# Kernel optimization log

Hardware: AMD Instinct MI355X
Metric: run time of the kernel (lower is better)

Reference implementation:

```python
import jax, jax.numpy as jnp
import numpy as np

D_MODEL = 1024
D_FFN = 4096
H = 16
D_HEAD = D_MODEL // H
B, L = 2, 2048
EPS = 1e-6


def layer_norm(x, a, b):
    # Matches torch: std is unbiased (ddof=1), and divides by (std + eps)
    mean = jnp.mean(x, axis=-1, keepdims=True)
    var = jnp.sum((x - mean) ** 2, axis=-1, keepdims=True) / (x.shape[-1] - 1)
    std = jnp.sqrt(var)
    return (x - mean) / (std + EPS) * a + b


def setup_inputs() -> dict:
    key = jax.random.key(0)
    ks = jax.random.split(key, 10)
    s = 0.02
    x = jax.random.normal(ks[0], (B, L, D_MODEL), dtype=jnp.float32)
    mask = jnp.tril(jnp.ones((L, L), dtype=jnp.int32))[None, None]  # causal [1,1,L,L]
    return {
        "x": x,
        "mask": mask,
        "Wqkv": jax.random.normal(ks[1], (D_MODEL, 3 * D_MODEL), jnp.float32) * s,
        "bqkv": jnp.zeros((3 * D_MODEL,), jnp.float32),
        "Wo": jax.random.normal(ks[2], (D_MODEL, D_MODEL), jnp.float32) * s,
        "bo": jnp.zeros((D_MODEL,), jnp.float32),
        "W1": jax.random.normal(ks[3], (D_MODEL, D_FFN), jnp.float32) * s,
        "b1": jnp.zeros((D_FFN,), jnp.float32),
        "W2": jax.random.normal(ks[4], (D_FFN, D_MODEL), jnp.float32) * s,
        "b2": jnp.zeros((D_MODEL,), jnp.float32),
        "ln1_a": jnp.ones((D_MODEL,), jnp.float32),
        "ln1_b": jnp.zeros((D_MODEL,), jnp.float32),
        "ln2_a": jnp.ones((D_MODEL,), jnp.float32),
        "ln2_b": jnp.zeros((D_MODEL,), jnp.float32),
    }


def reference(x, mask, Wqkv, bqkv, Wo, bo, W1, b1, W2, b2, ln1_a, ln1_b, ln2_a, ln2_b):
    b, l, d = x.shape
    # --- attention sublayer ---
    qkv = x @ Wqkv + bqkv                                   # [b, l, 3*d]
    qkv = qkv.reshape(b, l, 3, H, D_HEAD)                   # '(three h d)' ordering
    q, k, v = qkv[:, :, 0], qkv[:, :, 1], qkv[:, :, 2]      # each [b, l, h, dh]
    scores = jnp.einsum('bqhd,bkhd->bhqk', q, k) / jnp.sqrt(
        jnp.asarray(D_HEAD, x.dtype))                        # [b, h, lq, lk]
    scores = jnp.where(mask == 0, -jnp.inf, scores)
    p = jax.nn.softmax(scores, axis=-1)
    attn = jnp.einsum('bhqk,bkhd->bqhd', p, v).reshape(b, l, d)
    attn_out = attn @ Wo + bo
    x = layer_norm(x + attn_out, ln1_a, ln1_b)
    # --- MLP sublayer ---
    h = jax.nn.relu(x @ W1 + b1)
    mlp_out = h @ W2 + b2
    return layer_norm(x + mlp_out, ln2_a, ln2_b)
```

## Files before the change

kernel.cpp:

```cpp
#include <hip/hip_runtime.h>

#define D_MODEL 1024
#define D_FFN   4096
#define NH      16
#define DH      64
#define BB      2
#define LL      2048
#define MROWS   (BB * LL)

typedef unsigned short u16;
typedef unsigned int   u32;
typedef short bf16x8 __attribute__((ext_vector_type(8)));
typedef float f32x4  __attribute__((ext_vector_type(4)));

__device__ __forceinline__ float bf2f(u16 u) {
    union { u32 i; float f; } v;
    v.i = ((u32)u) << 16;
    return v.f;
}
__device__ __forceinline__ u16 f2bf(float f) {
    union { float f; u32 i; } v;
    v.f = f;
    u32 x = v.i;
    x += 0x7fffu + ((x >> 16) & 1u);
    return (u16)(x >> 16);
}
__device__ __forceinline__ float wave_sum(float v) {
    #pragma unroll
    for (int o = 32; o > 0; o >>= 1) v += __shfl_xor(v, o, 64);
    return v;
}
__device__ __forceinline__ u32 pack_bf_trunc(float a, float b) {
    return __builtin_amdgcn_perm(__float_as_uint(b), __float_as_uint(a),
                                 0x07060302u);
}

typedef const __attribute__((address_space(1))) u32 gu32;
typedef __attribute__((address_space(3))) u32 lu32;
__device__ __forceinline__ void gload_lds16(const void* g, void* l) {
    __builtin_amdgcn_global_load_lds((gu32*)g, (lu32*)l, 16, 0, 0);
}

__global__ __launch_bounds__(256) void cvt_kernel(
    const float* __restrict__ in, u16* __restrict__ out, int n)
{
    int i = (blockIdx.x * 256 + threadIdx.x) * 8;
    if (i >= n) return;
    float4 a = *(const float4*)(in + i);
    float4 b = *(const float4*)(in + i + 4);
    u16 o[8] = {f2bf(a.x), f2bf(a.y), f2bf(a.z), f2bf(a.w),
                f2bf(b.x), f2bf(b.y), f2bf(b.z), f2bf(b.w)};
    *(uint4*)(out + i) = *(const uint4*)o;
}

__global__ __launch_bounds__(256) void wt_kernel(
    const float* __restrict__ W, u16* __restrict__ Wt, int K, int N)
{
    __shared__ float tile[64][65];
    const int tid = threadIdx.x;
    const int n0 = blockIdx.x * 64;
    const int k0 = blockIdx.y * 64;

    int kr = tid >> 4;
    int nc = (tid & 15) * 4;
    #pragma unroll
    for (int p = 0; p < 4; ++p) {
        float4 v = *(const float4*)&W[(size_t)(k0 + kr + p * 16) * N + n0 + nc];
        tile[kr + p * 16][nc + 0] = v.x;
        tile[kr + p * 16][nc + 1] = v.y;
        tile[kr + p * 16][nc + 2] = v.z;
        tile[kr + p * 16][nc + 3] = v.w;
    }
    __syncthreads();

    int nr = tid >> 2;
    int kc = (tid & 3) * 16;
    u16 o[16];
    #pragma unroll
    for (int j = 0; j < 16; ++j) o[j] = f2bf(tile[kc + j][nr]);
    u16* dst = &Wt[(size_t)(n0 + nr) * K + k0 + kc];
    *(uint4*)dst       = *(const uint4*)&o[0];
    *(uint4*)(dst + 8) = *(const uint4*)&o[8];
}

template <int EPI, int RF32, int OF32, int KS>
__global__ __launch_bounds__(256) void gemm_bt_kernel(
    const u16* __restrict__ A, const u16* __restrict__ Bt,
    const float* __restrict__ bias, const void* __restrict__ resv,
    void* __restrict__ out0v, u16* __restrict__ out1, u16* __restrict__ out2,
    int M, int N, int K)
{
    __shared__ u16 sA[128 * 64];
    __shared__ u16 sB[128 * 64];

    const int tid  = threadIdx.x;
    const int lane = tid & 63;
    const int wave = tid >> 6;
    const int wm   = (wave & 1) * 64;
    const int wn   = (wave >> 1) * 64;
    const int quad = lane >> 4;
    const int l16  = lane & 15;

    const int nb  = gridDim.x;
    const int mb  = gridDim.y;
    const int f   = blockIdx.y * nb + blockIdx.x;
    const int xcd = f & 7;
    const int idx = f >> 3;
    const int rn  = nb >> 1;
    const int rm  = mb >> 2;
    const int n0  = ((xcd & 1) * rn + (idx % rn)) * 128;
    const int ym  = (xcd >> 1) * rm + (idx / rn);

    int s, m0;
    if (KS > 1) {
        const int mt = mb / KS;
        s  = ym / mt;
        m0 = (ym % mt) * 128;
    } else {
        s  = 0;
        m0 = ym * 128;
    }
    const int Kseg = K / KS;
    const int kbeg = s * Kseg;

    f32x4 acc[4][4];
    #pragma unroll
    for (int i = 0; i < 4; ++i)
        #pragma unroll
        for (int j = 0; j < 4; ++j)
            acc[i][j] = (f32x4){0.f, 0.f, 0.f, 0.f};

    const u16* Ablk = A  + (size_t)m0 * K;
    const u16* Bblk = Bt + (size_t)n0 * K;

    for (int k0 = kbeg; k0 < kbeg + Kseg; k0 += 64) {
        #pragma unroll
        for (int i = 0; i < 4; ++i) {
            int chunk = (i * 4 + wave) * 64 + lane;
            int r = chunk >> 3;
            int c = (chunk & 7) ^ (r & 7);
            size_t goff = (size_t)r * K + k0 + c * 8;
            gload_lds16(Ablk + goff, &sA[(i * 4 + wave) * 512]);
            gload_lds16(Bblk + goff, &sB[(i * 4 + wave) * 512]);
        }
        __syncthreads();

        #pragma unroll
        for (int ks = 0; ks < 2; ++ks) {
            bf16x8 af[4], bfr[4];
            #pragma unroll
            for (int i = 0; i < 4; ++i) {
                int R = wm + i * 16 + l16;
                int slot = R * 8 + ((ks * 4 + quad) ^ (R & 7));
                af[i] = *(const bf16x8*)&sA[slot * 8];
            }
            #pragma unroll
            for (int j = 0; j < 4; ++j) {
                int R = wn + j * 16 + l16;
                int slot = R * 8 + ((ks * 4 + quad) ^ (R & 7));
                bfr[j] = *(const bf16x8*)&sB[slot * 8];
            }
            #pragma unroll
            for (int i = 0; i < 4; ++i)
                #pragma unroll
                for (int j = 0; j < 4; ++j)
                    acc[i][j] = __builtin_amdgcn_mfma_f32_16x16x32_bf16(
                        af[i], bfr[j], acc[i][j], 0, 0, 0);
        }
        __syncthreads();
    }

    #pragma unroll
    for (int i = 0; i < 4; ++i) {
        int rowb = m0 + wm + i * 16 + quad * 4;
        #pragma unroll
        for (int j = 0; j < 4; ++j) {
            int col = n0 + wn + j * 16 + l16;
            float bv = (EPI == 3) ? 0.f : bias[col];
            #pragma unroll
            for (int r = 0; r < 4; ++r) {
                int rr = rowb + r;
                float v = acc[i][j][r] + bv;
                if (EPI == 0) {
                    int which = col >> 10;
                    int h     = (col >> 6) & 15;
                    int d     = col & 63;
                    int b     = rr >> 11;
                    int l     = rr & 2047;
                    size_t idx2 = ((size_t)(b * NH + h) * LL + l) * DH + d;
                    u16* o0 = (u16*)out0v;
                    if (which == 0)      o0[idx2]   = f2bf(v * 0.125f);
                    else if (which == 1) out1[idx2] = f2bf(v);
                    else                 out2[idx2] = f2bf(v);
                } else if (EPI == 3) {
                    ((u16*)out0v)[((size_t)s * M + rr) * N + col] = f2bf(v);
                } else {
                    size_t idx2 = (size_t)rr * N + col;
                    if (EPI == 1) {
                        v += RF32 ? ((const float*)resv)[idx2]
                                  : bf2f(((const u16*)resv)[idx2]);
                    } else {
                        v = v > 0.f ? v : 0.f;
                    }
                    if (OF32) ((float*)out0v)[idx2] = v;
                    else      ((u16*)out0v)[idx2]   = f2bf(v);
                }
            }
        }
    }
}

__global__ __launch_bounds__(256) void reduce4_kernel(
    const u16* __restrict__ P, const float* __restrict__ bias,
    const u16* __restrict__ res, float* __restrict__ out)
{
    const size_t SL = (size_t)MROWS * D_MODEL;
    size_t i = ((size_t)blockIdx.x * 256 + threadIdx.x) * 8;
    int col = (int)(i & (D_MODEL - 1));

    uint4 p0 = *(const uint4*)(P + i);
    uint4 p1 = *(const uint4*)(P + SL + i);
    uint4 p2 = *(const uint4*)(P + 2 * SL + i);
    uint4 p3 = *(const uint4*)(P + 3 * SL + i);
    uint4 rr = *(const uint4*)(res + i);
    float4 b0 = *(const float4*)(bias + col);
    float4 b1 = *(const float4*)(bias + col + 4);

    const u32* w0 = (const u32*)&p0;
    const u32* w1 = (const u32*)&p1;
    const u32* w2 = (const u32*)&p2;
    const u32* w3 = (const u32*)&p3;
    const u32* wr = (const u32*)&rr;
    float o[8];
    #pragma unroll
    for (int e = 0; e < 8; ++e) {
        int dw = e >> 1, sh = (e & 1) * 16;
        float v = bf2f((u16)(w0[dw] >> sh)) + bf2f((u16)(w1[dw] >> sh))
                + bf2f((u16)(w2[dw] >> sh)) + bf2f((u16)(w3[dw] >> sh))
                + bf2f((u16)(wr[dw] >> sh));
        o[e] = v;
    }
    o[0] += b0.x; o[1] += b0.y; o[2] += b0.z; o[3] += b0.w;
    o[4] += b1.x; o[5] += b1.y; o[6] += b1.z; o[7] += b1.w;
    *(float4*)(out + i)     = (float4){o[0], o[1], o[2], o[3]};
    *(float4*)(out + i + 4) = (float4){o[4], o[5], o[6], o[7]};
}

__global__ __launch_bounds__(256) void attn_kernel(
    const u16* __restrict__ Q, const u16* __restrict__ K,
    const u16* __restrict__ V, u16* __restrict__ out)
{
    __shared__ u16 ks[64 * 72];
    __shared__ u16 vs[64 * 72];
    __shared__ u16 ps[4][16 * 72];

    const int tid  = threadIdx.x;
    const int lane = tid & 63;
    const int wave = tid >> 6;
    const int l16  = lane & 15;
    const int quad = lane >> 4;

    const int f   = blockIdx.x;
    const int xcd = f & 7;
    const int idx = f >> 3;
    const int bh  = xcd * 4 + (idx >> 4);
    const int pr  = idx & 15;
    const int b   = bh >> 4, h = bh & 15;
    const size_t head_off = (size_t)bh * LL * DH;

    const u16* Qh = Q + head_off;
    const u16* Kh = K + head_off;
    const u16* Vh = V + head_off;

    const int qtA = 31 - pr, qtB = pr;
    const int baseA = qtA * 64 + wave * 16;
    const int baseB = qtB * 64 + wave * 16;
    const int qgA   = baseA + l16;
    const int qgB   = baseB + l16;

    const bf16x8 qfA0 = *(const bf16x8*)&Qh[(size_t)qgA * DH + quad * 8];
    const bf16x8 qfA1 = *(const bf16x8*)&Qh[(size_t)qgA * DH + 32 + quad * 8];
    const bf16x8 qfB0 = *(const bf16x8*)&Qh[(size_t)qgB * DH + quad * 8];
    const bf16x8 qfB1 = *(const bf16x8*)&Qh[(size_t)qgB * DH + 32 + quad * 8];

    float lA = 0.f, lB = 0.f;
    f32x4 oA[4], oB[4];
    #pragma unroll
    for (int t = 0; t < 4; ++t) {
        oA[t] = (f32x4){0.f, 0.f, 0.f, 0.f};
        oB[t] = (f32x4){0.f, 0.f, 0.f, 0.f};
    }

    u16* psw = &ps[wave][0];

    for (int c = 0; c <= qtA; ++c) {
        const bool doB = (c <= qtB);
        __syncthreads();
        {
            int key  = tid >> 2;
            int dim0 = (tid & 3) * 16;
            const u16* src = Kh + (size_t)(c * 64 + key) * DH + dim0;
            *(uint4*)&ks[key * 72 + dim0]     = *(const uint4*)src;
            *(uint4*)&ks[key * 72 + dim0 + 8] = *(const uint4*)(src + 8);
        }
        {
            int kp   = tid >> 3;
            int dim0 = (tid & 7) * 8;
            const u16* src = Vh + (size_t)(c * 64 + 2 * kp) * DH + dim0;
            uint4 v0 = *(const uint4*)src;
            uint4 v1 = *(const uint4*)(src + DH);
            const u32* w0 = (const u32*)&v0;
            const u32* w1 = (const u32*)&v1;
            #pragma unroll
            for (int e = 0; e < 8; ++e) {
                int d = dim0 + e;
                u32 lo = (w0[e >> 1] >> ((e & 1) * 16)) & 0xffffu;
                u32 hi = (w1[e >> 1] >> ((e & 1) * 16)) & 0xffffu;
                int csw = kp ^ (4 * ((d >> 3) & 7));
                *(u32*)&vs[d * 72 + 2 * csw] = lo | (hi << 16);
            }
        }
        __syncthreads();

        f32x4 stA[4], stB[4];
        #pragma unroll
        for (int t = 0; t < 4; ++t) {
            bf16x8 k0 = *(const bf16x8*)&ks[(t * 16 + l16) * 72 + quad * 8];
            bf16x8 k1 = *(const bf16x8*)&ks[(t * 16 + l16) * 72 + 32 + quad * 8];
            f32x4 s = (f32x4){0.f, 0.f, 0.f, 0.f};
            s = __builtin_amdgcn_mfma_f32_16x16x32_bf16(k0, qfA0, s, 0, 0, 0);
            s = __builtin_amdgcn_mfma_f32_16x16x32_bf16(k1, qfA1, s, 0, 0, 0);
            stA[t] = s;
            if (doB) {
                f32x4 s2 = (f32x4){0.f, 0.f, 0.f, 0.f};
                s2 = __builtin_amdgcn_mfma_f32_16x16x32_bf16(k0, qfB0, s2, 0, 0, 0);
                s2 = __builtin_amdgcn_mfma_f32_16x16x32_bf16(k1, qfB1, s2, 0, 0, 0);
                stB[t] = s2;
            }
        }

        if (c == qtA) {
            #pragma unroll
            for (int t = 0; t < 4; ++t)
                #pragma unroll
                for (int r = 0; r < 4; ++r)
                    if (c * 64 + t * 16 + quad * 4 + r > qgA) stA[t][r] = -INFINITY;
        }
        if (doB && c == qtB) {
            #pragma unroll
            for (int t = 0; t < 4; ++t)
                #pragma unroll
                for (int r = 0; r < 4; ++r)
                    if (c * 64 + t * 16 + quad * 4 + r > qgB) stB[t][r] = -INFINITY;
        }

        {
            float psum = 0.f;
            u32 pk[8];
            #pragma unroll
            for (int t = 0; t < 4; ++t) {
                float p0 = __expf(stA[t][0]), p1 = __expf(stA[t][1]);
                float p2 = __expf(stA[t][2]), p3 = __expf(stA[t][3]);
                psum += (p0 + p1) + (p2 + p3);
                pk[2 * t]     = pack_bf_trunc(p0, p1);
                pk[2 * t + 1] = pack_bf_trunc(p2, p3);
            }
            psum += __shfl_xor(psum, 16, 64);
            psum += __shfl_xor(psum, 32, 64);
            lA += psum;
            #pragma unroll
            for (int t = 0; t < 4; ++t) {
                uint2 w = {pk[2 * t], pk[2 * t + 1]};
                *(uint2*)&psw[l16 * 72 + t * 16 + quad * 4] = w;
            }
            bf16x8 pf0 = *(const bf16x8*)&psw[l16 * 72 + quad * 8];
            bf16x8 pf1 = *(const bf16x8*)&psw[l16 * 72 + 32 + quad * 8];
            #pragma unroll
            for (int dt = 0; dt < 4; ++dt) {
                int d  = dt * 16 + l16;
                int sw = 4 * ((d >> 3) & 7);
                bf16x8 vf0 = *(const bf16x8*)&vs[d * 72 + 2 * ((quad * 4) ^ sw)];
                bf16x8 vf1 = *(const bf16x8*)&vs[d * 72 + 2 * ((16 + quad * 4) ^ sw)];
                oA[dt] = __builtin_amdgcn_mfma_f32_16x16x32_bf16(pf0, vf0, oA[dt], 0, 0, 0);
                oA[dt] = __builtin_amdgcn_mfma_f32_16x16x32_bf16(pf1, vf1, oA[dt], 0, 0, 0);
            }
        }
        if (doB) {
            float psum = 0.f;
            u32 pk[8];
            #pragma unroll
            for (int t = 0; t < 4; ++t) {
                float p0 = __expf(stB[t][0]), p1 = __expf(stB[t][1]);
                float p2 = __expf(stB[t][2]), p3 = __expf(stB[t][3]);
                psum += (p0 + p1) + (p2 + p3);
                pk[2 * t]     = pack_bf_trunc(p0, p1);
                pk[2 * t + 1] = pack_bf_trunc(p2, p3);
            }
            psum += __shfl_xor(psum, 16, 64);
            psum += __shfl_xor(psum, 32, 64);
            lB += psum;
            #pragma unroll
            for (int t = 0; t < 4; ++t) {
                uint2 w = {pk[2 * t], pk[2 * t + 1]};
                *(uint2*)&psw[l16 * 72 + t * 16 + quad * 4] = w;
            }
            bf16x8 pf0 = *(const bf16x8*)&psw[l16 * 72 + quad * 8];
            bf16x8 pf1 = *(const bf16x8*)&psw[l16 * 72 + 32 + quad * 8];
            #pragma unroll
            for (int dt = 0; dt < 4; ++dt) {
                int d  = dt * 16 + l16;
                int sw = 4 * ((d >> 3) & 7);
                bf16x8 vf0 = *(const bf16x8*)&vs[d * 72 + 2 * ((quad * 4) ^ sw)];
                bf16x8 vf1 = *(const bf16x8*)&vs[d * 72 + 2 * ((16 + quad * 4) ^ sw)];
                oB[dt] = __builtin_amdgcn_mfma_f32_16x16x32_bf16(pf0, vf0, oB[dt], 0, 0, 0);
                oB[dt] = __builtin_amdgcn_mfma_f32_16x16x32_bf16(pf1, vf1, oB[dt], 0, 0, 0);
            }
        }
    }

    {
        float i0 = 1.f / __shfl(lA, quad * 4 + 0, 64);
        float i1 = 1.f / __shfl(lA, quad * 4 + 1, 64);
        float i2 = 1.f / __shfl(lA, quad * 4 + 2, 64);
        float i3 = 1.f / __shfl(lA, quad * 4 + 3, 64);
        #pragma unroll
        for (int dt = 0; dt < 4; ++dt) {
            size_t col = h * DH + dt * 16 + l16;
            size_t r0  = ((size_t)b * LL + baseA + quad * 4) * D_MODEL + col;
            out[r0]               = f2bf(oA[dt][0] * i0);
            out[r0 + D_MODEL]     = f2bf(oA[dt][1] * i1);
            out[r0 + 2 * D_MODEL] = f2bf(oA[dt][2] * i2);
            out[r0 + 3 * D_MODEL] = f2bf(oA[dt][3] * i3);
        }
    }
    {
        float i0 = 1.f / __shfl(lB, quad * 4 + 0, 64);
        float i1 = 1.f / __shfl(lB, quad * 4 + 1, 64);
        float i2 = 1.f / __shfl(lB, quad * 4 + 2, 64);
        float i3 = 1.f / __shfl(lB, quad * 4 + 3, 64);
        #pragma unroll
        for (int dt = 0; dt < 4; ++dt) {
            size_t col = h * DH + dt * 16 + l16;
            size_t r0  = ((size_t)b * LL + baseB + quad * 4) * D_MODEL + col;
            out[r0]               = f2bf(oB[dt][0] * i0);
            out[r0 + D_MODEL]     = f2bf(oB[dt][1] * i1);
            out[r0 + 2 * D_MODEL] = f2bf(oB[dt][2] * i2);
            out[r0 + 3 * D_MODEL] = f2bf(oB[dt][3] * i3);
        }
    }
}

template <int OF32>
__global__ __launch_bounds__(256) void ln_kernel(
    const float* __restrict__ t, const float* __restrict__ ga,
    const float* __restrict__ gb, void* __restrict__ outv)
{
    __shared__ float red[8];
    const int tid  = threadIdx.x;
    const int lane = tid & 63;
    const int wave = tid >> 6;
    const size_t row = blockIdx.x;

    const float* tr = t + row * D_MODEL;
    float4 u = *(const float4*)(tr + tid * 4);
    float x0 = u.x, x1 = u.y, x2 = u.z, x3 = u.w;

    float s = wave_sum(x0 + x1 + x2 + x3);
    if (lane == 0) red[wave] = s;
    __syncthreads();
    float mean = (red[0] + red[1] + red[2] + red[3]) * (1.f / 1024.f);

    float d0 = x0 - mean, d1 = x1 - mean, d2 = x2 - mean, d3 = x3 - mean;
    float v = wave_sum(d0 * d0 + d1 * d1 + d2 * d2 + d3 * d3);
    if (lane == 0) red[4 + wave] = v;
    __syncthreads();
    float var = (red[4] + red[5] + red[6] + red[7]) * (1.f / 1023.f);
    float inv = 1.f / (sqrtf(var) + 1e-6f);

    int c = tid * 4;
    float y0 = d0 * inv * ga[c + 0] + gb[c + 0];
    float y1 = d1 * inv * ga[c + 1] + gb[c + 1];
    float y2 = d2 * inv * ga[c + 2] + gb[c + 2];
    float y3 = d3 * inv * ga[c + 3] + gb[c + 3];
    if (OF32) {
        float4 y = {y0, y1, y2, y3};
        *(float4*)((float*)outv + row * D_MODEL + c) = y;
    } else {
        ushort4 y = {f2bf(y0), f2bf(y1), f2bf(y2), f2bf(y3)};
        *(ushort4*)((u16*)outv + row * D_MODEL + c) = y;
    }
}

extern "C" void kernel_launch(void* const* d_in, const int* in_sizes, int n_in,
                              void* d_out, int out_size, void* d_ws, size_t ws_size,
                              hipStream_t stream)
{
    const float* x    = (const float*)d_in[0];
    const float* Wqkv = (const float*)d_in[2];
    const float* bqkv = (const float*)d_in[3];
    const float* Wo   = (const float*)d_in[4];
    const float* bo   = (const float*)d_in[5];
    const float* W1   = (const float*)d_in[6];
    const float* b1   = (const float*)d_in[7];
    const float* W2   = (const float*)d_in[8];
    const float* b2   = (const float*)d_in[9];
    const float* ln1a = (const float*)d_in[10];
    const float* ln1b = (const float*)d_in[11];
    const float* ln2a = (const float*)d_in[12];
    const float* ln2b = (const float*)d_in[13];

    char* ws = (char*)d_ws;
    const size_t HSZ = (size_t)BB * NH * LL * DH;
    const size_t RSZ = (size_t)MROWS * D_MODEL;
    u16*   Qp    = (u16*)ws;
    u16*   Kp    = Qp + HSZ;
    u16*   Vp    = Kp + HSZ;
    u16*   attn  = Vp + HSZ;
    u16*   hbuf  = (u16*)ws;
    float* t1    = (float*)(ws + 33554432);
    u16*   xb    = (u16*)t1;
    u16*   x1    = (u16*)(ws + 50331648);
    u16*   Wqkvt = (u16*)(ws + 58720256);
    u16*   Wot   = (u16*)(ws + 65011712);
    u16*   W1t   = (u16*)(ws + 67108864);
    u16*   W2t   = (u16*)(ws + 75497472);
    u16*   Pbuf  = (u16*)(ws + 83886080);
    float* t2    = t1;

    dim3 blk(256);

    cvt_kernel<<<dim3(RSZ / 2048), blk, 0, stream>>>(x, xb, (int)RSZ);
    wt_kernel<<<dim3(48, 16), blk, 0, stream>>>(Wqkv, Wqkvt, D_MODEL, 3 * D_MODEL);
    wt_kernel<<<dim3(16, 16), blk, 0, stream>>>(Wo,   Wot,   D_MODEL, D_MODEL);
    wt_kernel<<<dim3(64, 16), blk, 0, stream>>>(W1,   W1t,   D_MODEL, D_FFN);
    wt_kernel<<<dim3(16, 64), blk, 0, stream>>>(W2,   W2t,   D_FFN,   D_MODEL);

    gemm_bt_kernel<0,0,0,1><<<dim3(24, 32), blk, 0, stream>>>(
        xb, Wqkvt, bqkv, nullptr, Qp, Kp, Vp, MROWS, 3 * D_MODEL, D_MODEL);
    attn_kernel<<<dim3(512), blk, 0, stream>>>(Qp, Kp, Vp, attn);
    gemm_bt_kernel<1,1,1,1><<<dim3(8, 32), blk, 0, stream>>>(
        attn, Wot, bo, x, t1, nullptr, nullptr, MROWS, D_MODEL, D_MODEL);
    ln_kernel<0><<<dim3(MROWS), blk, 0, stream>>>(t1, ln1a, ln1b, x1);
    gemm_bt_kernel<2,0,0,1><<<dim3(32, 32), blk, 0, stream>>>(
        x1, W1t, b1, nullptr, hbuf, nullptr, nullptr, MROWS, D_FFN, D_MODEL);
    gemm_bt_kernel<3,0,0,4><<<dim3(8, 128), blk, 0, stream>>>(
        hbuf, W2t, b2, nullptr, Pbuf, nullptr, nullptr, MROWS, D_MODEL, D_FFN);
    reduce4_kernel<<<dim3(RSZ / 2048), blk, 0, stream>>>(Pbuf, b2, x1, t2);
    ln_kernel<1><<<dim3(MROWS), blk, 0, stream>>>(t2, ln2a, ln2b, d_out);
}
```

Baseline: 366.2 us.

## Prefetch K/V tiles in attention, interleave PV MFMAs, split-K the Wo GEMM

```diff
diff --git a/kernel.cpp b/kernel.cpp
--- a/kernel.cpp
+++ b/kernel.cpp
@@ -210,38 +210,43 @@
     }
 }
 
-__global__ __launch_bounds__(256) void reduce4_kernel(
+template <int KS, int RF32>
+__global__ __launch_bounds__(256) void reduceK_kernel(
     const u16* __restrict__ P, const float* __restrict__ bias,
-    const u16* __restrict__ res, float* __restrict__ out)
+    const void* __restrict__ resv, float* __restrict__ out)
 {
     const size_t SL = (size_t)MROWS * D_MODEL;
     size_t i = ((size_t)blockIdx.x * 256 + threadIdx.x) * 8;
     int col = (int)(i & (D_MODEL - 1));
 
-    uint4 p0 = *(const uint4*)(P + i);
-    uint4 p1 = *(const uint4*)(P + SL + i);
-    uint4 p2 = *(const uint4*)(P + 2 * SL + i);
-    uint4 p3 = *(const uint4*)(P + 3 * SL + i);
-    uint4 rr = *(const uint4*)(res + i);
-    float4 b0 = *(const float4*)(bias + col);
-    float4 b1 = *(const float4*)(bias + col + 4);
-
-    const u32* w0 = (const u32*)&p0;
-    const u32* w1 = (const u32*)&p1;
-    const u32* w2 = (const u32*)&p2;
-    const u32* w3 = (const u32*)&p3;
-    const u32* wr = (const u32*)&rr;
     float o[8];
-    #pragma unroll
-    for (int e = 0; e < 8; ++e) {
-        int dw = e >> 1, sh = (e & 1) * 16;
-        float v = bf2f((u16)(w0[dw] >> sh)) + bf2f((u16)(w1[dw] >> sh))
-                + bf2f((u16)(w2[dw] >> sh)) + bf2f((u16)(w3[dw] >> sh))
-                + bf2f((u16)(wr[dw] >> sh));
-        o[e] = v;
-    }
-    o[0] += b0.x; o[1] += b0.y; o[2] += b0.z; o[3] += b0.w;
-    o[4] += b1.x; o[5] += b1.y; o[6] += b1.z; o[7] += b1.w;
+    {
+        float4 b0 = *(const float4*)(bias + col);
+        float4 b1 = *(const float4*)(bias + col + 4);
+        o[0] = b0.x; o[1] = b0.y; o[2] = b0.z; o[3] = b0.w;
+        o[4] = b1.x; o[5] = b1.y; o[6] = b1.z; o[7] = b1.w;
+    }
+    #pragma unroll
+    for (int s = 0; s < KS; ++s) {
+        uint4 p = *(const uint4*)(P + s * SL + i);
+        const u32* w = (const u32*)&p;
+        #pragma unroll
+        for (int e = 0; e < 8; ++e)
+            o[e] += bf2f((u16)(w[e >> 1] >> ((e & 1) * 16)));
+    }
+    if (RF32) {
+        const float* res = (const float*)resv;
+        float4 r0 = *(const float4*)(res + i);
+        float4 r1 = *(const float4*)(res + i + 4);
+        o[0] += r0.x; o[1] += r0.y; o[2] += r0.z; o[3] += r0.w;
+        o[4] += r1.x; o[5] += r1.y; o[6] += r1.z; o[7] += r1.w;
+    } else {
+        uint4 rr = *(const uint4*)((const u16*)resv + i);
+        const u32* w = (const u32*)&rr;
+        #pragma unroll
+        for (int e = 0; e < 8; ++e)
+            o[e] += bf2f((u16)(w[e >> 1] >> ((e & 1) * 16)));
+    }
     *(float4*)(out + i)     = (float4){o[0], o[1], o[2], o[3]};
     *(float4*)(out + i + 4) = (float4){o[4], o[5], o[6], o[7]};
 }
@@ -252,7 +257,7 @@
 {
     __shared__ u16 ks[64 * 72];
     __shared__ u16 vs[64 * 72];
-    __shared__ u16 ps[4][16 * 72];
+    __shared__ u16 ps[4][2][16 * 72];
 
     const int tid  = threadIdx.x;
     const int lane = tid & 63;
@@ -291,29 +296,35 @@
         oB[t] = (f32x4){0.f, 0.f, 0.f, 0.f};
     }
 
-    u16* psw = &ps[wave][0];
+    u16* psA = &ps[wave][0][0];
+    u16* psB = &ps[wave][1][0];
+
+    const int key = tid >> 2;
+    const int kd0 = (tid & 3) * 16;
+    const int kp  = tid >> 3;
+    const int vd0 = (tid & 7) * 8;
+
+    uint4 kr0, kr1, vr0, vr1;
+    {
+        const u16* ksrc = Kh + (size_t)key * DH + kd0;
+        kr0 = *(const uint4*)ksrc;
+        kr1 = *(const uint4*)(ksrc + 8);
+        const u16* vsrc = Vh + (size_t)(2 * kp) * DH + vd0;
+        vr0 = *(const uint4*)vsrc;
+        vr1 = *(const uint4*)(vsrc + DH);
+    }
 
     for (int c = 0; c <= qtA; ++c) {
         const bool doB = (c <= qtB);
         __syncthreads();
+        *(uint4*)&ks[key * 72 + kd0]     = kr0;
+        *(uint4*)&ks[key * 72 + kd0 + 8] = kr1;
         {
-            int key  = tid >> 2;
-            int dim0 = (tid & 3) * 16;
-            const u16* src = Kh + (size_t)(c * 64 + key) * DH + dim0;
-            *(uint4*)&ks[key * 72 + dim0]     = *(const uint4*)src;
-            *(uint4*)&ks[key * 72 + dim0 + 8] = *(const uint4*)(src + 8);
-        }
-        {
-            int kp   = tid >> 3;
-            int dim0 = (tid & 7) * 8;
-            const u16* src = Vh + (size_t)(c * 64 + 2 * kp) * DH + dim0;
-            uint4 v0 = *(const uint4*)src;
-            uint4 v1 = *(const uint4*)(src + DH);
-            const u32* w0 = (const u32*)&v0;
-            const u32* w1 = (const u32*)&v1;
+            const u32* w0 = (const u32*)&vr0;
+            const u32* w1 = (const u32*)&vr1;
             #pragma unroll
             for (int e = 0; e < 8; ++e) {
-                int d = dim0 + e;
+                int d = vd0 + e;
                 u32 lo = (w0[e >> 1] >> ((e & 1) * 16)) & 0xffffu;
                 u32 hi = (w1[e >> 1] >> ((e & 1) * 16)) & 0xffffu;
                 int csw = kp ^ (4 * ((d >> 3) & 7));
@@ -321,6 +332,14 @@
             }
         }
         __syncthreads();
+        if (c < qtA) {
+            const u16* ksrc = Kh + (size_t)((c + 1) * 64 + key) * DH + kd0;
+            kr0 = *(const uint4*)ksrc;
+            kr1 = *(const uint4*)(ksrc + 8);
+            const u16* vsrc = Vh + (size_t)((c + 1) * 64 + 2 * kp) * DH + vd0;
+            vr0 = *(const uint4*)vsrc;
+            vr1 = *(const uint4*)(vsrc + DH);
+        }
 
         f32x4 stA[4], stB[4];
         #pragma unroll
@@ -356,64 +375,52 @@
 
         {
             float psum = 0.f;
-            u32 pk[8];
             #pragma unroll
             for (int t = 0; t < 4; ++t) {
                 float p0 = __expf(stA[t][0]), p1 = __expf(stA[t][1]);
                 float p2 = __expf(stA[t][2]), p3 = __expf(stA[t][3]);
                 psum += (p0 + p1) + (p2 + p3);
-                pk[2 * t]     = pack_bf_trunc(p0, p1);
-                pk[2 * t + 1] = pack_bf_trunc(p2, p3);
+                uint2 w = {pack_bf_trunc(p0, p1), pack_bf_trunc(p2, p3)};
+                *(uint2*)&psA[l16 * 72 + t * 16 + quad * 4] = w;
             }
             psum += __shfl_xor(psum, 16, 64);
             psum += __shfl_xor(psum, 32, 64);
             lA += psum;
-            #pragma unroll
-            for (int t = 0; t < 4; ++t) {
-                uint2 w = {pk[2 * t], pk[2 * t + 1]};
-                *(uint2*)&psw[l16 * 72 + t * 16 + quad * 4] = w;
-            }
-            bf16x8 pf0 = *(const bf16x8*)&psw[l16 * 72 + quad * 8];
-            bf16x8 pf1 = *(const bf16x8*)&psw[l16 * 72 + 32 + quad * 8];
-            #pragma unroll
-            for (int dt = 0; dt < 4; ++dt) {
-                int d  = dt * 16 + l16;
-                int sw = 4 * ((d >> 3) & 7);
-                bf16x8 vf0 = *(const bf16x8*)&vs[d * 72 + 2 * ((quad * 4) ^ sw)];
-                bf16x8 vf1 = *(const bf16x8*)&vs[d * 72 + 2 * ((16 + quad * 4) ^ sw)];
-                oA[dt] = __builtin_amdgcn_mfma_f32_16x16x32_bf16(pf0, vf0, oA[dt], 0, 0, 0);
-                oA[dt] = __builtin_amdgcn_mfma_f32_16x16x32_bf16(pf1, vf1, oA[dt], 0, 0, 0);
-            }
         }
         if (doB) {
             float psum = 0.f;
-            u32 pk[8];
             #pragma unroll
             for (int t = 0; t < 4; ++t) {
                 float p0 = __expf(stB[t][0]), p1 = __expf(stB[t][1]);
                 float p2 = __expf(stB[t][2]), p3 = __expf(stB[t][3]);
                 psum += (p0 + p1) + (p2 + p3);
-                pk[2 * t]     = pack_bf_trunc(p0, p1);
-                pk[2 * t + 1] = pack_bf_trunc(p2, p3);
+                uint2 w = {pack_bf_trunc(p0, p1), pack_bf_trunc(p2, p3)};
+                *(uint2*)&psB[l16 * 72 + t * 16 + quad * 4] = w;
             }
             psum += __shfl_xor(psum, 16, 64);
             psum += __shfl_xor(psum, 32, 64);
             lB += psum;
-            #pragma unroll
-            for (int t = 0; t < 4; ++t) {
-                uint2 w = {pk[2 * t], pk[2 * t + 1]};
-                *(uint2*)&psw[l16 * 72 + t * 16 + quad * 4] = w;
-            }
-            bf16x8 pf0 = *(const bf16x8*)&psw[l16 * 72 + quad * 8];
-            bf16x8 pf1 = *(const bf16x8*)&psw[l16 * 72 + 32 + quad * 8];
-            #pragma unroll
-            for (int dt = 0; dt < 4; ++dt) {
-                int d  = dt * 16 + l16;
-                int sw = 4 * ((d >> 3) & 7);
-                bf16x8 vf0 = *(const bf16x8*)&vs[d * 72 + 2 * ((quad * 4) ^ sw)];
-                bf16x8 vf1 = *(const bf16x8*)&vs[d * 72 + 2 * ((16 + quad * 4) ^ sw)];
-                oB[dt] = __builtin_amdgcn_mfma_f32_16x16x32_bf16(pf0, vf0, oB[dt], 0, 0, 0);
-                oB[dt] = __builtin_amdgcn_mfma_f32_16x16x32_bf16(pf1, vf1, oB[dt], 0, 0, 0);
+        }
+
+        bf16x8 pfA0 = *(const bf16x8*)&psA[l16 * 72 + quad * 8];
+        bf16x8 pfA1 = *(const bf16x8*)&psA[l16 * 72 + 32 + quad * 8];
+        bf16x8 pfB0, pfB1;
+        if (doB) {
+            pfB0 = *(const bf16x8*)&psB[l16 * 72 + quad * 8];
+            pfB1 = *(const bf16x8*)&psB[l16 * 72 + 32 + quad * 8];
+        }
+
+        #pragma unroll
+        for (int dt = 0; dt < 4; ++dt) {
+            int d  = dt * 16 + l16;
+            int sw = 4 * ((d >> 3) & 7);
+            bf16x8 vf0 = *(const bf16x8*)&vs[d * 72 + 2 * ((quad * 4) ^ sw)];
+            bf16x8 vf1 = *(const bf16x8*)&vs[d * 72 + 2 * ((16 + quad * 4) ^ sw)];
+            oA[dt] = __builtin_amdgcn_mfma_f32_16x16x32_bf16(pfA0, vf0, oA[dt], 0, 0, 0);
+            oA[dt] = __builtin_amdgcn_mfma_f32_16x16x32_bf16(pfA1, vf1, oA[dt], 0, 0, 0);
+            if (doB) {
+                oB[dt] = __builtin_amdgcn_mfma_f32_16x16x32_bf16(pfB0, vf0, oB[dt], 0, 0, 0);
+                oB[dt] = __builtin_amdgcn_mfma_f32_16x16x32_bf16(pfB1, vf1, oB[dt], 0, 0, 0);
             }
         }
     }
@@ -538,13 +545,14 @@
     gemm_bt_kernel<0,0,0,1><<<dim3(24, 32), blk, 0, stream>>>(
         xb, Wqkvt, bqkv, nullptr, Qp, Kp, Vp, MROWS, 3 * D_MODEL, D_MODEL);
     attn_kernel<<<dim3(512), blk, 0, stream>>>(Qp, Kp, Vp, attn);
-    gemm_bt_kernel<1,1,1,1><<<dim3(8, 32), blk, 0, stream>>>(
-        attn, Wot, bo, x, t1, nullptr, nullptr, MROWS, D_MODEL, D_MODEL);
+    gemm_bt_kernel<3,0,0,2><<<dim3(8, 64), blk, 0, stream>>>(
+        attn, Wot, bo, nullptr, Pbuf, nullptr, nullptr, MROWS, D_MODEL, D_MODEL);
+    reduceK_kernel<2,1><<<dim3(RSZ / 2048), blk, 0, stream>>>(Pbuf, bo, x, t1);
     ln_kernel<0><<<dim3(MROWS), blk, 0, stream>>>(t1, ln1a, ln1b, x1);
     gemm_bt_kernel<2,0,0,1><<<dim3(32, 32), blk, 0, stream>>>(
         x1, W1t, b1, nullptr, hbuf, nullptr, nullptr, MROWS, D_FFN, D_MODEL);
     gemm_bt_kernel<3,0,0,4><<<dim3(8, 128), blk, 0, stream>>>(
         hbuf, W2t, b2, nullptr, Pbuf, nullptr, nullptr, MROWS, D_MODEL, D_FFN);
-    reduce4_kernel<<<dim3(RSZ / 2048), blk, 0, stream>>>(Pbuf, b2, x1, t2);
+    reduceK_kernel<4,0><<<dim3(RSZ / 2048), blk, 0, stream>>>(Pbuf, b2, x1, t2);
     ln_kernel<1><<<dim3(MROWS), blk, 0, stream>>>(t2, ln2a, ln2b, d_out);
 }
```

Measured after the change: 367.8 us. About the same (+0.4%).
